# Kernel optimization log

Hardware: AMD Instinct MI355X
Metric: run time of the kernel (lower is better)

## Reference

```python
import jax, jax.numpy as jnp
import numpy as np
from jax import lax

C = 128
G = 8          # deformable groups
K = 3
KK = K * K
PAD = 1


def conv2d(x, w, pad):
    return lax.conv_general_dilated(
        x, w, window_strides=(1, 1), padding=((pad, pad), (pad, pad)),
        dimension_numbers=('NCHW', 'OIHW', 'NCHW'))


def deform_conv_v2(x, offset, mask, weight, bias):
    """Modulated deformable conv (DCNv2), stride=1, pad=1, dil=1.
    x:[B,C,H,W] offset:[B,2*G*KK,H,W] mask:[B,G*KK,H,W] weight:[O,C,K,K]."""
    B, Cin, H, W = x.shape
    Cg = Cin // G
    # CUDA kernel layout per group: [k0_y, k0_x, k1_y, k1_x, ...]
    off = offset.reshape(B, G, KK, 2, H, W)
    off_y, off_x = off[:, :, :, 0], off[:, :, :, 1]          # [B,G,KK,H,W]
    m = mask.reshape(B, G, KK, H, W)

    kyy, kxx = jnp.meshgrid(jnp.arange(K), jnp.arange(K), indexing='ij')
    kyy = kyy.reshape(KK).astype(x.dtype)
    kxx = kxx.reshape(KK).astype(x.dtype)
    yy = jnp.arange(H, dtype=x.dtype)
    xx = jnp.arange(W, dtype=x.dtype)
    # absolute sampling positions [B,G,KK,H,W]
    py = yy[None, None, None, :, None] - PAD + kyy[None, None, :, None, None] + off_y
    px = xx[None, None, None, None, :] - PAD + kxx[None, None, :, None, None] + off_x

    y0 = jnp.floor(py)
    x0 = jnp.floor(px)
    ly = py - y0
    lx = px - x0

    xg = x.reshape(B, G, Cg, H * W)

    def gather(yi, xi):
        valid = ((yi >= 0) & (yi <= H - 1) & (xi >= 0) & (xi <= W - 1)).astype(x.dtype)
        yc = jnp.clip(yi, 0, H - 1).astype(jnp.int32)
        xc = jnp.clip(xi, 0, W - 1).astype(jnp.int32)
        idx = (yc * W + xc).reshape(B, G, 1, KK * H * W)
        v = jnp.take_along_axis(xg, idx, axis=3).reshape(B, G, Cg, KK, H, W)
        return v * valid[:, :, None]

    val = (gather(y0, x0) * ((1 - ly) * (1 - lx))[:, :, None]
           + gather(y0, x0 + 1) * ((1 - ly) * lx)[:, :, None]
           + gather(y0 + 1, x0) * (ly * (1 - lx))[:, :, None]
           + gather(y0 + 1, x0 + 1) * (ly * lx)[:, :, None])
    val = val * m[:, :, None]                                # modulation

    w = weight.reshape(-1, G, Cg, KK)                        # [O,G,Cg,KK]
    out = jnp.einsum('bgckhw,ogck->bohw', val, w)
    return out + bias[None, :, None, None]


def setup_inputs() -> dict:
    key = jax.random.key(0)
    ks = jax.random.split(key, 7)
    B, H, W = 4, 128, 128
    feat_l = jax.random.normal(ks[0], (B, C, H, W), jnp.float32)
    feat_s = jax.random.normal(ks[1], (B, C, H // 2, W // 2), jnp.float32)
    # 1x1 offset conv (256 -> 128), bias=False
    W_off = jax.random.normal(ks[2], (C, 2 * C, 1, 1), jnp.float32) * (1.0 / np.sqrt(2 * C))
    # conv_offset_mask: 128 -> G*3*KK = 216, 3x3, bias=True (zero-init in practice; small random here)
    W_om = jax.random.normal(ks[3], (G * 3 * KK, C, K, K), jnp.float32) * 0.01
    b_om = jax.random.normal(ks[4], (G * 3 * KK,), jnp.float32) * 0.01
    # DCN weight 128 -> 128, 3x3
    W_dcn = jax.random.normal(ks[5], (C, C, K, K), jnp.float32) * (1.0 / np.sqrt(C * KK))
    b_dcn = jax.random.normal(ks[6], (C,), jnp.float32) * 0.01
    return {'feat_l': feat_l, 'feat_s': feat_s, 'W_off': W_off,
            'W_om': W_om, 'b_om': b_om, 'W_dcn': W_dcn, 'b_dcn': b_dcn}


def reference(feat_l, feat_s, W_off, W_om, b_om, W_dcn, b_dcn):
    B, Cc, H, W = feat_l.shape
    # F.interpolate bilinear align_corners=False == jax.image.resize bilinear
    feat_up = jax.image.resize(feat_s, (B, Cc, H, W), method='bilinear')
    offset_feat = conv2d(jnp.concatenate([feat_l, feat_up * 2], axis=1), W_off, pad=0)
    om = conv2d(offset_feat, W_om, pad=1) + b_om[None, :, None, None]
    o1, o2, mask = jnp.split(om, 3, axis=1)
    offset = jnp.concatenate([o1, o2], axis=1)
    mask = jax.nn.sigmoid(mask)
    feat_align = jax.nn.relu(deform_conv_v2(feat_up, offset, mask, W_dcn, b_dcn))
    return feat_align + feat_l
```

## Files before the change

kernel.cpp:

```cpp
#include <hip/hip_runtime.h>
#include <hip/hip_bf16.h>
#include <math.h>

#define BB 4
#define CC 128
#define HH 128
#define WW 128
#define HWs 16384
#define GG 8
#define OMCH 216

typedef __bf16 bf16_t;
typedef bf16_t bf16x8 __attribute__((ext_vector_type(8)));
typedef float f32x4 __attribute__((ext_vector_type(4)));
typedef float f32x2 __attribute__((ext_vector_type(2), aligned(4)));

__global__ __launch_bounds__(256) void k_prep(const float* __restrict__ W_off,
                                              const float* __restrict__ W_om,
                                              const float* __restrict__ W_dcn,
                                              bf16_t* __restrict__ wpack1,
                                              bf16_t* __restrict__ wpack,
                                              bf16_t* __restrict__ wpdcn) {
    int idx = blockIdx.x * 256 + threadIdx.x;
    if (idx < 4096) {
        int j = idx;
        int lane = j & 63;
        int rest = j >> 6;
        int ot = rest & 7;
        int ks = rest >> 3;
        int o = ot * 16 + (lane & 15);
        int cbase = ks * 32 + ((lane >> 4) << 3);
        bf16x8 v;
        #pragma unroll
        for (int r = 0; r < 8; ++r) v[r] = (bf16_t)W_off[o * 256 + cbase + r];
        *((bf16x8*)wpack1 + j) = v;
    } else if (idx < 4096 + 36864) {
        int j = idx - 4096;
        int lane = j & 63;
        int rest = j >> 6;
        int ot = rest & 15;
        int ks = rest >> 4;
        int cblk = ks / 9, tap = ks % 9;
        int o = ot * 16 + (lane & 15);
        int cbase = cblk * 32 + ((lane >> 4) << 3);
        bf16x8 v;
        #pragma unroll
        for (int r = 0; r < 8; ++r) {
            float x = (o < OMCH) ? W_om[((o * 128 + cbase + r) * 9) + tap] : 0.0f;
            v[r] = (bf16_t)x;
        }
        *((bf16x8*)wpack + j) = v;
    } else if (idx < 4096 + 36864 + 20480) {
        int j = idx - 40960;
        int lane = j & 63;
        int rest = j >> 6;
        int ot = rest & 7;
        int gks = rest >> 3;
        int g = gks / 5, ks = gks % 5;
        int o = ot * 16 + (lane & 15);
        int Kbase = ks * 32 + ((lane >> 4) << 3);
        bf16x8 v;
        #pragma unroll
        for (int r = 0; r < 8; ++r) {
            int K = Kbase + r;
            float x = 0.0f;
            if (K < 144) {
                int tap = K >> 4, cpp = K & 15;
                x = W_dcn[((o * 128) + g * 16 + cpp) * 9 + tap];
            }
            v[r] = (bf16_t)x;
        }
        *((bf16x8*)wpdcn + j) = v;
    }
}

__global__ __launch_bounds__(256) void k_upsample(const float* __restrict__ fs,
                                                  float* __restrict__ fu) {
    int idx = blockIdx.x * 256 + threadIdx.x;
    int x = idx & 127, y = (idx >> 7) & 127, bc = idx >> 14;
    int j = y >> 1, i = x >> 1;
    int ya, yb; float wya, wyb;
    if (y & 1) { ya = j; yb = (j < 63) ? j + 1 : 63; wya = 0.75f; wyb = 0.25f; }
    else       { ya = (j > 0) ? j - 1 : 0; yb = j;   wya = 0.25f; wyb = 0.75f; }
    int xa, xb; float wxa, wxb;
    if (x & 1) { xa = i; xb = (i < 63) ? i + 1 : 63; wxa = 0.75f; wxb = 0.25f; }
    else       { xa = (i > 0) ? i - 1 : 0; xb = i;   wxa = 0.25f; wxb = 0.75f; }
    const float* p = fs + (size_t)bc * 4096;
    float v = wya * (wxa * p[ya * 64 + xa] + wxb * p[ya * 64 + xb])
            + wyb * (wxa * p[yb * 64 + xa] + wxb * p[yb * 64 + xb]);
    fu[idx] = v;
}

#define X1LD 264
__global__ __launch_bounds__(256) void k_conv1m(const float* __restrict__ fl,
                                                const float* __restrict__ fu,
                                                const bf16_t* __restrict__ wp1,
                                                float* __restrict__ outp) {
    __shared__ __align__(16) bf16_t X[64][X1LD];
    int t = threadIdx.x, lane = t & 63, w = t >> 6;
    int b = blockIdx.x >> 8;
    int pos0 = (blockIdx.x & 255) << 6;
    f32x4 acc[2][4];
    #pragma unroll
    for (int i = 0; i < 2; ++i)
        #pragma unroll
        for (int j = 0; j < 4; ++j)
            acc[i][j] = (f32x4){0.f, 0.f, 0.f, 0.f};
    #pragma unroll 4
    for (int it = 0; it < 32; ++it) {
        int cp = it * 4 + w;
        int c = cp * 2;
        float v0, v1;
        if (c < 128) {
            size_t gb = (size_t)(b * 128 + c) * HWs + pos0 + lane;
            v0 = fl[gb]; v1 = fl[gb + HWs];
        } else {
            size_t gb = (size_t)(b * 128 + (c - 128)) * HWs + pos0 + lane;
            v0 = 2.0f * fu[gb]; v1 = 2.0f * fu[gb + HWs];
        }
        X[lane][c] = (bf16_t)v0;
        X[lane][c + 1] = (bf16_t)v1;
    }
    __syncthreads();
    #pragma unroll
    for (int ks = 0; ks < 8; ++ks) {
        bf16x8 af[2], bfr[4];
        const bf16x8* wp = (const bf16x8*)wp1 + ((ks * 8 + w * 2) * 64 + lane);
        af[0] = wp[0];
        af[1] = wp[64];
        #pragma unroll
        for (int pi = 0; pi < 4; ++pi)
            bfr[pi] = *(const bf16x8*)&X[pi * 16 + (lane & 15)][ks * 32 + ((lane >> 4) << 3)];
        #pragma unroll
        for (int oi = 0; oi < 2; ++oi)
            #pragma unroll
            for (int pi = 0; pi < 4; ++pi)
                acc[oi][pi] = __builtin_amdgcn_mfma_f32_16x16x32_bf16(af[oi], bfr[pi], acc[oi][pi], 0, 0, 0);
    }
    #pragma unroll
    for (int oi = 0; oi < 2; ++oi) {
        int obase = (w * 2 + oi) * 16 + ((lane >> 4) << 2);
        #pragma unroll
        for (int j = 0; j < 4; ++j) {
            int o = obase + j;
            size_t ob = (size_t)(b * 128 + o) * HWs + pos0 + (lane & 15);
            #pragma unroll
            for (int pi = 0; pi < 4; ++pi)
                outp[ob + pi * 16] = acc[oi][pi][j];
        }
    }
}

#define X3LD 40
__global__ __launch_bounds__(256) void k_conv3m(const float* __restrict__ A,
                                                const bf16_t* __restrict__ wpack,
                                                const float* __restrict__ bom,
                                                float* __restrict__ om) {
    __shared__ __align__(16) bf16_t Xs[3 * 66 * X3LD];
    int t = threadIdx.x;
    int lane = t & 63, w = t >> 6;
    int b = blockIdx.x >> 8;
    int pos0 = (blockIdx.x & 255) << 6;
    int y = pos0 >> 7, x0 = pos0 & 127;
    f32x4 acc[4][4];
    #pragma unroll
    for (int i = 0; i < 4; ++i)
        #pragma unroll
        for (int j = 0; j < 4; ++j)
            acc[i][j] = (f32x4){0.f, 0.f, 0.f, 0.f};

    for (int cblk = 0; cblk < 4; ++cblk) {
        __syncthreads();
        for (int id = t; id < 3168; id += 256) {
            int col = id % 66;
            int rest = id / 66;
            int dy = rest % 3;
            int cp = rest / 3;
            int gy = y - 1 + dy, gx = x0 - 1 + col;
            float v0 = 0.f, v1 = 0.f;
            if ((unsigned)gy < 128u && (unsigned)gx < 128u) {
                size_t gb = ((size_t)(b * 128 + cblk * 32 + cp * 2) * 128 + gy) * 128 + gx;
                v0 = A[gb];
                v1 = A[gb + HWs];
            }
            int le = (dy * 66 + col) * X3LD + cp * 2;
            Xs[le] = (bf16_t)v0;
            Xs[le + 1] = (bf16_t)v1;
        }
        __syncthreads();
        #pragma unroll
        for (int tap = 0; tap < 9; ++tap) {
            const int ky = tap / 3, kx = tap % 3;
            bf16x8 af[4], bfr[4];
            const bf16x8* wp = (const bf16x8*)wpack + ((size_t)((cblk * 9 + tap) * 16 + w * 4) * 64 + lane);
            #pragma unroll
            for (int oi = 0; oi < 4; ++oi) af[oi] = wp[oi * 64];
            #pragma unroll
            for (int pi = 0; pi < 4; ++pi) {
                int colb = pi * 16 + (lane & 15) + kx;
                bfr[pi] = *(const bf16x8*)&Xs[(ky * 66 + colb) * X3LD + ((lane >> 4) << 3)];
            }
            #pragma unroll
            for (int oi = 0; oi < 4; ++oi)
                #pragma unroll
                for (int pi = 0; pi < 4; ++pi)
                    acc[oi][pi] = __builtin_amdgcn_mfma_f32_16x16x32_bf16(af[oi], bfr[pi], acc[oi][pi], 0, 0, 0);
        }
    }
    #pragma unroll
    for (int oi = 0; oi < 4; ++oi) {
        int obase = (w * 4 + oi) * 16 + ((lane >> 4) << 2);
        #pragma unroll
        for (int j = 0; j < 4; ++j) {
            int o = obase + j;
            if (o < OMCH) {
                float bv = bom[o];
                size_t ob = (size_t)(b * OMCH + o) * HWs + pos0 + (lane & 15);
                #pragma unroll
                for (int pi = 0; pi < 4; ++pi) {
                    float v = acc[oi][pi][j] + bv;
                    if (o >= 144) v = 1.0f / (1.0f + expf(-v));
                    om[ob + pi * 16] = v;
                }
            }
        }
    }
}

__global__ __launch_bounds__(512, 4) void k_dcn(const float* __restrict__ fu,
                                                const float* __restrict__ om,
                                                const bf16_t* __restrict__ wpd,
                                                const float* __restrict__ bdcn,
                                                const float* __restrict__ fl,
                                                float* __restrict__ outp) {
    __shared__ __align__(16) bf16_t val[2][64][168];
    int t = threadIdx.x;
    int lane = t & 63, w = t >> 6;
    int b = blockIdx.x >> 8;
    int pos0 = (blockIdx.x & 255) << 6;
    int y = pos0 >> 7, x0 = pos0 & 127;
    f32x4 acc[4];
    #pragma unroll
    for (int j = 0; j < 4; ++j) acc[j] = (f32x4){0.f, 0.f, 0.f, 0.f};
    for (int id = t; id < 2 * 64 * 24; id += 512) {
        int bufg = id / 1536, r = id % 1536;
        val[bufg][r / 24][144 + (r % 24)] = (bf16_t)0.0f;
    }

    const float* omb = om + (size_t)b * OMCH * HWs;
    const float* fub = fu + (size_t)b * 128 * HWs;
    size_t sp = (size_t)y * 128 + x0 + lane;

    const int u1gl = (w + 8) / 9, u1tap = (w + 8) % 9;
    const int u2tap = w + 7;

    auto process_unit = [&](int gl, int g, int tap, float oy, float ox, float m)
        __attribute__((always_inline)) {
        int ky = tap / 3, kx = tap % 3;
        int x = x0 + lane;
        float py = (float)(y - 1 + ky) + oy;
        float px = (float)(x - 1 + kx) + ox;
        float fy0 = floorf(py), fx0 = floorf(px);
        float ly = py - fy0, lx = px - fx0;
        int y0 = (int)fy0, x0i = (int)fx0;
        float vy0 = ((unsigned)y0 < 128u) ? 1.0f : 0.0f;
        float vy1 = ((unsigned)(y0 + 1) < 128u) ? 1.0f : 0.0f;
        float vx0 = ((unsigned)x0i < 128u) ? 1.0f : 0.0f;
        float vx1 = ((unsigned)(x0i + 1) < 128u) ? 1.0f : 0.0f;
        int yc0 = min(max(y0, 0), 127), yc1 = min(max(y0 + 1, 0), 127);
        int xc0 = min(max(x0i, 0), 127), xc1 = min(max(x0i + 1, 0), 127);
        float pw00 = (1.0f - ly) * (1.0f - lx) * m * vy0 * vx0;
        float pw01 = (1.0f - ly) * lx * m * vy0 * vx1;
        float pw10 = ly * (1.0f - lx) * m * vy1 * vx0;
        float pw11 = ly * lx * m * vy1 * vx1;
        int xr = min(xc0, 126);
        int s0 = xc0 - xr, s1 = xc1 - xr;
        float ax = (s0 ? 0.0f : pw00) + (s1 ? 0.0f : pw01);
        float ay = (s0 ? pw00 : 0.0f) + (s1 ? pw01 : 0.0f);
        float bx = (s0 ? 0.0f : pw10) + (s1 ? 0.0f : pw11);
        float by = (s0 ? pw10 : 0.0f) + (s1 ? pw11 : 0.0f);
        int a_lo = yc0 * 128 + xr;
        int a_hi = yc1 * 128 + xr;
        const float* bp = fub + (size_t)(g * 16) * HWs;
        #pragma unroll
        for (int half = 0; half < 2; ++half) {
            bf16x8 ov;
            #pragma unroll
            for (int q = 0; q < 2; ++q) {
                f32x2 ra[4], rb[4];
                #pragma unroll
                for (int c = 0; c < 4; ++c) {
                    const float* p = bp + (size_t)(half * 8 + q * 4 + c) * HWs;
                    ra[c] = *(const f32x2*)(p + a_lo);
                    rb[c] = *(const f32x2*)(p + a_hi);
                }
                #pragma unroll
                for (int c = 0; c < 4; ++c) {
                    float v = ax * ra[c][0] + ay * ra[c][1] + bx * rb[c][0] + by * rb[c][1];
                    ov[q * 4 + c] = (bf16_t)v;
                }
            }
            *(bf16x8*)&val[gl][lane][tap * 16 + half * 8] = ov;
        }
    };

    float oy0, ox0, m0, oy1, ox1, m1, oy2 = 0.f, ox2 = 0.f, m2 = 0.f;
    {
        int g0 = 0, u1g = u1gl, u2g = 1;
        oy0 = omb[(size_t)(g0 * 18 + w * 2) * HWs + sp];
        ox0 = omb[(size_t)(g0 * 18 + w * 2 + 1) * HWs + sp];
        m0  = omb[(size_t)(144 + g0 * 9 + w) * HWs + sp];
        oy1 = omb[(size_t)(u1g * 18 + u1tap * 2) * HWs + sp];
        ox1 = omb[(size_t)(u1g * 18 + u1tap * 2 + 1) * HWs + sp];
        m1  = omb[(size_t)(144 + u1g * 9 + u1tap) * HWs + sp];
        if (w < 2) {
            oy2 = omb[(size_t)(u2g * 18 + u2tap * 2) * HWs + sp];
            ox2 = omb[(size_t)(u2g * 18 + u2tap * 2 + 1) * HWs + sp];
            m2  = omb[(size_t)(144 + u2g * 9 + u2tap) * HWs + sp];
        }
    }

    for (int gc = 0; gc < 4; ++gc) {
        process_unit(0, gc * 2, w, oy0, ox0, m0);
        process_unit(u1gl, gc * 2 + u1gl, u1tap, oy1, ox1, m1);
        if (w < 2) process_unit(1, gc * 2 + 1, u2tap, oy2, ox2, m2);
        if (gc < 3) {
            int g0 = (gc + 1) * 2;
            int u1g = g0 + u1gl, u2g = g0 + 1;
            oy0 = omb[(size_t)(g0 * 18 + w * 2) * HWs + sp];
            ox0 = omb[(size_t)(g0 * 18 + w * 2 + 1) * HWs + sp];
            m0  = omb[(size_t)(144 + g0 * 9 + w) * HWs + sp];
            oy1 = omb[(size_t)(u1g * 18 + u1tap * 2) * HWs + sp];
            ox1 = omb[(size_t)(u1g * 18 + u1tap * 2 + 1) * HWs + sp];
            m1  = omb[(size_t)(144 + u1g * 9 + u1tap) * HWs + sp];
            if (w < 2) {
                oy2 = omb[(size_t)(u2g * 18 + u2tap * 2) * HWs + sp];
                ox2 = omb[(size_t)(u2g * 18 + u2tap * 2 + 1) * HWs + sp];
                m2  = omb[(size_t)(144 + u2g * 9 + u2tap) * HWs + sp];
            }
        }
        __syncthreads();
        #pragma unroll
        for (int gl = 0; gl < 2; ++gl) {
            int g = gc * 2 + gl;
            #pragma unroll
            for (int ks = 0; ks < 5; ++ks) {
                bf16x8 af = *((const bf16x8*)wpd + (((g * 5 + ks) * 8 + w) * 64 + lane));
                #pragma unroll
                for (int pi = 0; pi < 4; ++pi) {
                    bf16x8 bfr = *(const bf16x8*)&val[gl][pi * 16 + (lane & 15)][ks * 32 + ((lane >> 4) << 3)];
                    acc[pi] = __builtin_amdgcn_mfma_f32_16x16x32_bf16(af, bfr, acc[pi], 0, 0, 0);
                }
            }
        }
        __syncthreads();
    }
    #pragma unroll
    for (int j = 0; j < 4; ++j) {
        int o = w * 16 + ((lane >> 4) << 2) + j;
        float bv = bdcn[o];
        size_t base = (size_t)(b * 128 + o) * HWs + pos0 + (lane & 15);
        #pragma unroll
        for (int pi = 0; pi < 4; ++pi) {
            float v = fmaxf(acc[pi][j] + bv, 0.0f) + fl[base + pi * 16];
            outp[base + pi * 16] = v;
        }
    }
}

extern "C" void kernel_launch(void* const* d_in, const int* in_sizes, int n_in,
                              void* d_out, int out_size, void* d_ws, size_t ws_size,
                              hipStream_t stream) {
    const float* feat_l = (const float*)d_in[0];
    const float* feat_s = (const float*)d_in[1];
    const float* W_off  = (const float*)d_in[2];
    const float* W_om   = (const float*)d_in[3];
    const float* b_om   = (const float*)d_in[4];
    const float* W_dcn  = (const float*)d_in[5];
    const float* b_dcn  = (const float*)d_in[6];
    float* out = (float*)d_out;
    float* ws = (float*)d_ws;

    float* feat_up = ws;
    float* offs    = ws + 8388608;
    float* om      = ws + 16777216;
    bf16_t* wpack1 = (bf16_t*)(ws + 30932992);
    bf16_t* wpack  = (bf16_t*)(ws + 30949376);
    bf16_t* wpdcn  = (bf16_t*)(ws + 31096832);

    k_prep<<<240, 256, 0, stream>>>(W_off, W_om, W_dcn, wpack1, wpack, wpdcn);
    k_upsample<<<32768, 256, 0, stream>>>(feat_s, feat_up);
    k_conv1m<<<1024, 256, 0, stream>>>(feat_l, feat_up, wpack1, offs);
    k_conv3m<<<1024, 256, 0, stream>>>(offs, wpack, b_om, om);
    k_dcn<<<1024, 512, 0, stream>>>(feat_up, om, wpdcn, b_dcn, feat_l, out);
}
```

Baseline: 349.1 us.

## Store intermediates in bf16 and rebalance DCN sampling work across waves

The upsampled features, the offset conv output and the offset/mask tensor are now stored as bf16 rather than fp32, which halves the global traffic between the stages. The factor of 2 on the upsampled half of the input moves into the packed conv1 weights. The upsample kernel now writes two output pixels per thread. The DCN gather reads bf16 pairs through unaligned-safe 32-bit loads, and the leftover tap units are split by channel half across four waves instead of two. This trades some accuracy in offsets and sampled values for less memory bandwidth and better load balance.

Result: no change. 350.9 us (+0.5%).

```diff
diff --git a/kernel.cpp b/kernel.cpp
--- a/kernel.cpp
+++ b/kernel.cpp
@@ -11,9 +11,15 @@
 #define OMCH 216
 
 typedef __bf16 bf16_t;
+typedef unsigned int u32;
+typedef bf16_t bf16x2 __attribute__((ext_vector_type(2)));
+typedef bf16_t bf16x4 __attribute__((ext_vector_type(4)));
 typedef bf16_t bf16x8 __attribute__((ext_vector_type(8)));
 typedef float f32x4 __attribute__((ext_vector_type(4)));
-typedef float f32x2 __attribute__((ext_vector_type(2), aligned(4)));
+
+__device__ __forceinline__ float bf2f(u32 hword16) {
+    union { u32 u; float f; } t; t.u = hword16 << 16; return t.f;
+}
 
 __global__ __launch_bounds__(256) void k_prep(const float* __restrict__ W_off,
                                               const float* __restrict__ W_om,
@@ -32,7 +38,10 @@
         int cbase = ks * 32 + ((lane >> 4) << 3);
         bf16x8 v;
         #pragma unroll
-        for (int r = 0; r < 8; ++r) v[r] = (bf16_t)W_off[o * 256 + cbase + r];
+        for (int r = 0; r < 8; ++r) {
+            float s = (cbase + r >= 128) ? 2.0f : 1.0f;
+            v[r] = (bf16_t)(W_off[o * 256 + cbase + r] * s);
+        }
         *((bf16x8*)wpack1 + j) = v;
     } else if (idx < 4096 + 36864) {
         int j = idx - 4096;
@@ -75,27 +84,32 @@
 }
 
 __global__ __launch_bounds__(256) void k_upsample(const float* __restrict__ fs,
-                                                  float* __restrict__ fu) {
+                                                  bf16_t* __restrict__ fub) {
     int idx = blockIdx.x * 256 + threadIdx.x;
-    int x = idx & 127, y = (idx >> 7) & 127, bc = idx >> 14;
-    int j = y >> 1, i = x >> 1;
+    int i = idx & 63, y = (idx >> 6) & 127, bc = idx >> 13;
+    int j = y >> 1;
     int ya, yb; float wya, wyb;
     if (y & 1) { ya = j; yb = (j < 63) ? j + 1 : 63; wya = 0.75f; wyb = 0.25f; }
     else       { ya = (j > 0) ? j - 1 : 0; yb = j;   wya = 0.25f; wyb = 0.75f; }
-    int xa, xb; float wxa, wxb;
-    if (x & 1) { xa = i; xb = (i < 63) ? i + 1 : 63; wxa = 0.75f; wxb = 0.25f; }
-    else       { xa = (i > 0) ? i - 1 : 0; xb = i;   wxa = 0.25f; wxb = 0.75f; }
+    int im1 = (i > 0) ? i - 1 : 0;
+    int ip1 = (i < 63) ? i + 1 : 63;
     const float* p = fs + (size_t)bc * 4096;
-    float v = wya * (wxa * p[ya * 64 + xa] + wxb * p[ya * 64 + xb])
-            + wyb * (wxa * p[yb * 64 + xa] + wxb * p[yb * 64 + xb]);
-    fu[idx] = v;
+    float am = p[ya * 64 + im1], a0 = p[ya * 64 + i], ap = p[ya * 64 + ip1];
+    float bm = p[yb * 64 + im1], b0 = p[yb * 64 + i], bp = p[yb * 64 + ip1];
+    float rm = wya * am + wyb * bm;
+    float r0 = wya * a0 + wyb * b0;
+    float rp = wya * ap + wyb * bp;
+    bf16x2 o2;
+    o2[0] = (bf16_t)(0.25f * rm + 0.75f * r0);
+    o2[1] = (bf16_t)(0.75f * r0 + 0.25f * rp);
+    *(bf16x2*)&fub[(size_t)idx * 2] = o2;
 }
 
 #define X1LD 264
 __global__ __launch_bounds__(256) void k_conv1m(const float* __restrict__ fl,
-                                                const float* __restrict__ fu,
+                                                const bf16_t* __restrict__ fub,
                                                 const bf16_t* __restrict__ wp1,
-                                                float* __restrict__ outp) {
+                                                bf16_t* __restrict__ offs) {
     __shared__ __align__(16) bf16_t X[64][X1LD];
     int t = threadIdx.x, lane = t & 63, w = t >> 6;
     int b = blockIdx.x >> 8;
@@ -110,16 +124,15 @@
     for (int it = 0; it < 32; ++it) {
         int cp = it * 4 + w;
         int c = cp * 2;
-        float v0, v1;
         if (c < 128) {
             size_t gb = (size_t)(b * 128 + c) * HWs + pos0 + lane;
-            v0 = fl[gb]; v1 = fl[gb + HWs];
+            X[lane][c] = (bf16_t)fl[gb];
+            X[lane][c + 1] = (bf16_t)fl[gb + HWs];
         } else {
             size_t gb = (size_t)(b * 128 + (c - 128)) * HWs + pos0 + lane;
-            v0 = 2.0f * fu[gb]; v1 = 2.0f * fu[gb + HWs];
-        }
-        X[lane][c] = (bf16_t)v0;
-        X[lane][c + 1] = (bf16_t)v1;
+            X[lane][c] = fub[gb];
+            X[lane][c + 1] = fub[gb + HWs];
+        }
     }
     __syncthreads();
     #pragma unroll
@@ -146,16 +159,16 @@
             size_t ob = (size_t)(b * 128 + o) * HWs + pos0 + (lane & 15);
             #pragma unroll
             for (int pi = 0; pi < 4; ++pi)
-                outp[ob + pi * 16] = acc[oi][pi][j];
+                offs[ob + pi * 16] = (bf16_t)acc[oi][pi][j];
         }
     }
 }
 
 #define X3LD 40
-__global__ __launch_bounds__(256) void k_conv3m(const float* __restrict__ A,
+__global__ __launch_bounds__(256) void k_conv3m(const bf16_t* __restrict__ A,
                                                 const bf16_t* __restrict__ wpack,
                                                 const float* __restrict__ bom,
-                                                float* __restrict__ om) {
+                                                bf16_t* __restrict__ om) {
     __shared__ __align__(16) bf16_t Xs[3 * 66 * X3LD];
     int t = threadIdx.x;
     int lane = t & 63, w = t >> 6;
@@ -177,15 +190,15 @@
             int dy = rest % 3;
             int cp = rest / 3;
             int gy = y - 1 + dy, gx = x0 - 1 + col;
-            float v0 = 0.f, v1 = 0.f;
+            bf16_t v0 = (bf16_t)0.f, v1 = (bf16_t)0.f;
             if ((unsigned)gy < 128u && (unsigned)gx < 128u) {
                 size_t gb = ((size_t)(b * 128 + cblk * 32 + cp * 2) * 128 + gy) * 128 + gx;
                 v0 = A[gb];
                 v1 = A[gb + HWs];
             }
             int le = (dy * 66 + col) * X3LD + cp * 2;
-            Xs[le] = (bf16_t)v0;
-            Xs[le + 1] = (bf16_t)v1;
+            Xs[le] = v0;
+            Xs[le + 1] = v1;
         }
         __syncthreads();
         #pragma unroll
@@ -220,15 +233,15 @@
                 for (int pi = 0; pi < 4; ++pi) {
                     float v = acc[oi][pi][j] + bv;
                     if (o >= 144) v = 1.0f / (1.0f + expf(-v));
-                    om[ob + pi * 16] = v;
+                    om[ob + pi * 16] = (bf16_t)v;
                 }
             }
         }
     }
 }
 
-__global__ __launch_bounds__(512, 4) void k_dcn(const float* __restrict__ fu,
-                                                const float* __restrict__ om,
+__global__ __launch_bounds__(512, 4) void k_dcn(const bf16_t* __restrict__ fub,
+                                                const bf16_t* __restrict__ om,
                                                 const bf16_t* __restrict__ wpd,
                                                 const float* __restrict__ bdcn,
                                                 const float* __restrict__ fl,
@@ -247,15 +260,16 @@
         val[bufg][r / 24][144 + (r % 24)] = (bf16_t)0.0f;
     }
 
-    const float* omb = om + (size_t)b * OMCH * HWs;
-    const float* fub = fu + (size_t)b * 128 * HWs;
+    const bf16_t* omb = om + (size_t)b * OMCH * HWs;
+    const bf16_t* fb  = fub + (size_t)b * 128 * HWs;
     size_t sp = (size_t)y * 128 + x0 + lane;
 
     const int u1gl = (w + 8) / 9, u1tap = (w + 8) % 9;
-    const int u2tap = w + 7;
-
-    auto process_unit = [&](int gl, int g, int tap, float oy, float ox, float m)
-        __attribute__((always_inline)) {
+    const int u2tap = 7 + (w >> 1);
+    const int u2c0 = (w & 1) * 8;
+
+    auto process_range = [&](int gl, int g, int tap, float oy, float ox, float m,
+                             int ch0, int nch) __attribute__((always_inline)) {
         int ky = tap / 3, kx = tap % 3;
         int x = x0 + lane;
         float py = (float)(y - 1 + ky) + oy;
@@ -279,64 +293,66 @@
         float ay = (s0 ? pw00 : 0.0f) + (s1 ? pw01 : 0.0f);
         float bx = (s0 ? 0.0f : pw10) + (s1 ? 0.0f : pw11);
         float by = (s0 ? pw10 : 0.0f) + (s1 ? pw11 : 0.0f);
-        int a_lo = yc0 * 128 + xr;
-        int a_hi = yc1 * 128 + xr;
-        const float* bp = fub + (size_t)(g * 16) * HWs;
-        #pragma unroll
-        for (int half = 0; half < 2; ++half) {
-            bf16x8 ov;
-            #pragma unroll
-            for (int q = 0; q < 2; ++q) {
-                f32x2 ra[4], rb[4];
-                #pragma unroll
-                for (int c = 0; c < 4; ++c) {
-                    const float* p = bp + (size_t)(half * 8 + q * 4 + c) * HWs;
-                    ra[c] = *(const f32x2*)(p + a_lo);
-                    rb[c] = *(const f32x2*)(p + a_hi);
-                }
-                #pragma unroll
-                for (int c = 0; c < 4; ++c) {
-                    float v = ax * ra[c][0] + ay * ra[c][1] + bx * rb[c][0] + by * rb[c][1];
-                    ov[q * 4 + c] = (bf16_t)v;
-                }
-            }
-            *(bf16x8*)&val[gl][lane][tap * 16 + half * 8] = ov;
+        int s = xr & 1;
+        int e_lo = yc0 * 128 + xr - s;
+        int e_hi = yc1 * 128 + xr - s;
+        const bf16_t* bp = fb + (size_t)(g * 16) * HWs;
+        for (int cb = 0; cb < nch; cb += 4) {
+            u32 alo[4], ahi[4], blo[4], bhi[4];
+            #pragma unroll
+            for (int c = 0; c < 4; ++c) {
+                const bf16_t* p = bp + (size_t)(ch0 + cb + c) * HWs;
+                alo[c] = *(const u32*)(p + e_lo);
+                ahi[c] = *(const u32*)(p + e_lo + 2);
+                blo[c] = *(const u32*)(p + e_hi);
+                bhi[c] = *(const u32*)(p + e_hi + 2);
+            }
+            bf16x4 ov;
+            #pragma unroll
+            for (int c = 0; c < 4; ++c) {
+                u32 ca = s ? ((alo[c] >> 16) | (ahi[c] << 16)) : alo[c];
+                u32 cbp = s ? ((blo[c] >> 16) | (bhi[c] << 16)) : blo[c];
+                float v = ax * bf2f(ca & 0xffffu) + ay * bf2f(ca >> 16)
+                        + bx * bf2f(cbp & 0xffffu) + by * bf2f(cbp >> 16);
+                ov[c] = (bf16_t)v;
+            }
+            *(bf16x4*)&val[gl][lane][tap * 16 + ch0 + cb] = ov;
         }
     };
 
     float oy0, ox0, m0, oy1, ox1, m1, oy2 = 0.f, ox2 = 0.f, m2 = 0.f;
     {
         int g0 = 0, u1g = u1gl, u2g = 1;
-        oy0 = omb[(size_t)(g0 * 18 + w * 2) * HWs + sp];
-        ox0 = omb[(size_t)(g0 * 18 + w * 2 + 1) * HWs + sp];
-        m0  = omb[(size_t)(144 + g0 * 9 + w) * HWs + sp];
-        oy1 = omb[(size_t)(u1g * 18 + u1tap * 2) * HWs + sp];
-        ox1 = omb[(size_t)(u1g * 18 + u1tap * 2 + 1) * HWs + sp];
-        m1  = omb[(size_t)(144 + u1g * 9 + u1tap) * HWs + sp];
-        if (w < 2) {
-            oy2 = omb[(size_t)(u2g * 18 + u2tap * 2) * HWs + sp];
-            ox2 = omb[(size_t)(u2g * 18 + u2tap * 2 + 1) * HWs + sp];
-            m2  = omb[(size_t)(144 + u2g * 9 + u2tap) * HWs + sp];
+        oy0 = (float)omb[(size_t)(g0 * 18 + w * 2) * HWs + sp];
+        ox0 = (float)omb[(size_t)(g0 * 18 + w * 2 + 1) * HWs + sp];
+        m0  = (float)omb[(size_t)(144 + g0 * 9 + w) * HWs + sp];
+        oy1 = (float)omb[(size_t)(u1g * 18 + u1tap * 2) * HWs + sp];
+        ox1 = (float)omb[(size_t)(u1g * 18 + u1tap * 2 + 1) * HWs + sp];
+        m1  = (float)omb[(size_t)(144 + u1g * 9 + u1tap) * HWs + sp];
+        if (w < 4) {
+            oy2 = (float)omb[(size_t)(u2g * 18 + u2tap * 2) * HWs + sp];
+            ox2 = (float)omb[(size_t)(u2g * 18 + u2tap * 2 + 1) * HWs + sp];
+            m2  = (float)omb[(size_t)(144 + u2g * 9 + u2tap) * HWs + sp];
         }
     }
 
     for (int gc = 0; gc < 4; ++gc) {
-        process_unit(0, gc * 2, w, oy0, ox0, m0);
-        process_unit(u1gl, gc * 2 + u1gl, u1tap, oy1, ox1, m1);
-        if (w < 2) process_unit(1, gc * 2 + 1, u2tap, oy2, ox2, m2);
+        process_range(0, gc * 2, w, oy0, ox0, m0, 0, 16);
+        process_range(u1gl, gc * 2 + u1gl, u1tap, oy1, ox1, m1, 0, 16);
+        if (w < 4) process_range(1, gc * 2 + 1, u2tap, oy2, ox2, m2, u2c0, 8);
         if (gc < 3) {
             int g0 = (gc + 1) * 2;
             int u1g = g0 + u1gl, u2g = g0 + 1;
-            oy0 = omb[(size_t)(g0 * 18 + w * 2) * HWs + sp];
-            ox0 = omb[(size_t)(g0 * 18 + w * 2 + 1) * HWs + sp];
-            m0  = omb[(size_t)(144 + g0 * 9 + w) * HWs + sp];
-            oy1 = omb[(size_t)(u1g * 18 + u1tap * 2) * HWs + sp];
-            ox1 = omb[(size_t)(u1g * 18 + u1tap * 2 + 1) * HWs + sp];
-            m1  = omb[(size_t)(144 + u1g * 9 + u1tap) * HWs + sp];
-            if (w < 2) {
-                oy2 = omb[(size_t)(u2g * 18 + u2tap * 2) * HWs + sp];
-                ox2 = omb[(size_t)(u2g * 18 + u2tap * 2 + 1) * HWs + sp];
-                m2  = omb[(size_t)(144 + u2g * 9 + u2tap) * HWs + sp];
+            oy0 = (float)omb[(size_t)(g0 * 18 + w * 2) * HWs + sp];
+            ox0 = (float)omb[(size_t)(g0 * 18 + w * 2 + 1) * HWs + sp];
+            m0  = (float)omb[(size_t)(144 + g0 * 9 + w) * HWs + sp];
+            oy1 = (float)omb[(size_t)(u1g * 18 + u1tap * 2) * HWs + sp];
+            ox1 = (float)omb[(size_t)(u1g * 18 + u1tap * 2 + 1) * HWs + sp];
+            m1  = (float)omb[(size_t)(144 + u1g * 9 + u1tap) * HWs + sp];
+            if (w < 4) {
+                oy2 = (float)omb[(size_t)(u2g * 18 + u2tap * 2) * HWs + sp];
+                ox2 = (float)omb[(size_t)(u2g * 18 + u2tap * 2 + 1) * HWs + sp];
+                m2  = (float)omb[(size_t)(144 + u2g * 9 + u2tap) * HWs + sp];
             }
         }
         __syncthreads();
@@ -381,16 +397,16 @@
     float* out = (float*)d_out;
     float* ws = (float*)d_ws;
 
-    float* feat_up = ws;
-    float* offs    = ws + 8388608;
-    float* om      = ws + 16777216;
-    bf16_t* wpack1 = (bf16_t*)(ws + 30932992);
-    bf16_t* wpack  = (bf16_t*)(ws + 30949376);
-    bf16_t* wpdcn  = (bf16_t*)(ws + 31096832);
+    bf16_t* fub    = (bf16_t*)ws;
+    bf16_t* offs   = (bf16_t*)(ws + 4194304);
+    bf16_t* om     = (bf16_t*)(ws + 8388608);
+    bf16_t* wpack1 = (bf16_t*)(ws + 15466496);
+    bf16_t* wpack  = (bf16_t*)(ws + 15482880);
+    bf16_t* wpdcn  = (bf16_t*)(ws + 15630336);
 
     k_prep<<<240, 256, 0, stream>>>(W_off, W_om, W_dcn, wpack1, wpack, wpdcn);
-    k_upsample<<<32768, 256, 0, stream>>>(feat_s, feat_up);
-    k_conv1m<<<1024, 256, 0, stream>>>(feat_l, feat_up, wpack1, offs);
+    k_upsample<<<16384, 256, 0, stream>>>(feat_s, fub);
+    k_conv1m<<<1024, 256, 0, stream>>>(feat_l, fub, wpack1, offs);
     k_conv3m<<<1024, 256, 0, stream>>>(offs, wpack, b_om, om);
-    k_dcn<<<1024, 512, 0, stream>>>(feat_up, om, wpdcn, b_dcn, feat_l, out);
-}
+    k_dcn<<<1024, 512, 0, stream>>>(fub, om, wpdcn, b_dcn, feat_l, out);
+}
```
